# Kernel optimization log

Measured on AMD Instinct MI355X. Metric: run time of the kernel, lower is better.

## Reference

```python
import jax, jax.numpy as jnp
import numpy as np

SCALES = (1, 3, 7, 15)
EPS_LN = 1e-5

def _layernorm(x, g, b):
    mu = jnp.mean(x, axis=-1, keepdims=True)
    var = jnp.mean(jnp.square(x - mu), axis=-1, keepdims=True)
    return (x - mu) / jnp.sqrt(var + EPS_LN) * g + b

def setup_inputs() -> dict:
    key = jax.random.key(0)
    ks = jax.random.split(key, 6)
    B, L, H, NL = 8, 4096, 1024, 4
    s = 0.02
    return {
        "sequence_features": jax.random.normal(ks[0], (B, L, H), jnp.float32),
        "hierarchy_masks": jax.random.uniform(ks[1], (B, L, NL), jnp.float32),
        "level_embeddings": jax.random.normal(ks[2], (NL, H), jnp.float32) * s,
        "lt_w": jax.random.normal(ks[3], (H, H), jnp.float32) * (1.0 / np.sqrt(H)),
        "lt_b": jnp.zeros((H,), jnp.float32),
        "ln1_g": jnp.ones((H,), jnp.float32),
        "ln1_b": jnp.zeros((H,), jnp.float32),
        "ft_w": jax.random.normal(ks[4], (H, H), jnp.float32) * (1.0 / np.sqrt(H)),
        "ft_b": jnp.zeros((H,), jnp.float32),
        "ln2_g": jnp.ones((H,), jnp.float32),
        "ln2_b": jnp.zeros((H,), jnp.float32),
    }

def _hierarchical_fusion(t, masks, level_emb, temperature=1.0):
    # t: [B,L,H], masks: [B,L,NL], level_emb: [NL,H]
    H = t.shape[-1]
    scores = jnp.einsum('blh,nh->bln', t, level_emb) / temperature      # [B,L,NL]
    keep = masks > 0.5
    w = jnp.where(keep, jnp.exp(scores), 0.0)                            # masked exp weights
    tot = jnp.sum(w, axis=-1, keepdims=True)                             # [B,L,1]
    fused = jnp.einsum('bln,nh->blh', w, level_emb)
    fused = jnp.where(tot > 1e-8, fused / jnp.where(tot > 1e-8, tot, 1.0), fused)
    gate = jax.nn.sigmoid(jnp.sum(fused * t, axis=-1, keepdims=True) / H)
    return gate * fused + (1.0 - gate) * t

def _multi_scale(x):
    # x: [B,L,H]; variable-window mean per scale via prefix sums
    B, L, H = x.shape
    csum = jnp.concatenate([jnp.zeros((B, 1, H), x.dtype), jnp.cumsum(x, axis=1)], axis=1)  # [B,L+1,H]
    pos = jnp.arange(L)
    agg = jnp.zeros_like(x)
    for scale in SCALES:
        start = jnp.clip(pos - scale // 2, 0, L)
        end = jnp.clip(pos + scale // 2 + 1, 0, L)
        wsum = jnp.take(csum, end, axis=1) - jnp.take(csum, start, axis=1)  # [B,L,H]
        cnt = (end - start).astype(x.dtype)[None, :, None]
        sw = 1.0 / (1.0 + np.log(float(scale)))
        agg = agg + sw * (wsum / cnt)
    return agg

def reference(sequence_features, hierarchy_masks, level_embeddings, lt_w, lt_b,
              ln1_g, ln1_b, ft_w, ft_b, ln2_g, ln2_b):
    t = _layernorm(sequence_features @ lt_w + lt_b, ln1_g, ln1_b)
    fused = _hierarchical_fusion(t, hierarchy_masks, level_embeddings)
    agg = _multi_scale(fused)
    out = _layernorm(agg @ ft_w + ft_b, ln2_g, ln2_b)
    return out + sequence_features
```

## Files before the change

### kernel.cpp

```cpp
#include <hip/hip_runtime.h>
#include <stdint.h>

typedef unsigned short u16;
typedef unsigned int u32;
typedef u16 u16x8 __attribute__((ext_vector_type(8)));
typedef u16 u16x4 __attribute__((ext_vector_type(4)));
typedef u16 u16x2 __attribute__((ext_vector_type(2)));
typedef __bf16 bf16x8 __attribute__((ext_vector_type(8)));
typedef float f32x4 __attribute__((ext_vector_type(4)));

__device__ __forceinline__ float bf2f(u16 u) {
    unsigned int x = ((unsigned int)u) << 16;
    float f; __builtin_memcpy(&f, &x, 4); return f;
}
__device__ __forceinline__ u16 f2bf(float f) {
    unsigned int x; __builtin_memcpy(&x, &f, 4);
    x += 0x7fffu + ((x >> 16) & 1u);
    return (u16)(x >> 16);
}
__device__ __forceinline__ float wsum(float v) {
#pragma unroll
    for (int o = 32; o > 0; o >>= 1) v += __shfl_xor(v, o, 64);
    return v;
}

__device__ __forceinline__ void gload16(const void* g, void* l) {
    const __attribute__((address_space(1))) u32* gp =
        reinterpret_cast<const __attribute__((address_space(1))) u32*>(
            reinterpret_cast<uintptr_t>(g));
    __attribute__((address_space(3))) u32* lp =
        reinterpret_cast<__attribute__((address_space(3))) u32*>(
            reinterpret_cast<uintptr_t>(l));
    __builtin_amdgcn_global_load_lds(gp, lp, 16, 0, 0);
}

template<int C_F32>
__global__ __launch_bounds__(256) void gemm_bt(
    const u16* __restrict__ A, const u16* __restrict__ Bt,
    void* __restrict__ Cp, int M, int N, int K)
{
    __shared__ __align__(16) u16 sA[128 * 32];
    __shared__ __align__(16) u16 sB[128 * 32];
    const int t = threadIdx.x;
    const int lane = t & 63, wave = t >> 6;
    const int quad = lane >> 4, lr = lane & 15;

    const int nwg = gridDim.x * gridDim.y;
    int id = blockIdx.y * gridDim.x + blockIdx.x;
    int swz = ((nwg & 7) == 0) ? ((id & 7) * (nwg >> 3) + (id >> 3)) : id;
    const int bx = swz % gridDim.x, by = swz / gridDim.x;
    const int m0 = by * 128, n0 = bx * 128;
    const int wm = (wave & 1) * 64, wn = (wave >> 1) * 64;

    const int r0 = t >> 2, kc = (t & 3) * 8;
    const u16* ga = A + (size_t)(m0 + r0) * K + kc;
    const u16* gb = Bt + (size_t)(n0 + r0) * K + kc;
    u16* la = sA + t * 8;
    u16* lb = sB + t * 8;
    const size_t rstride = (size_t)64 * K;

    f32x4 acc[4][4] = {};

    for (int kt = 0; kt < K; kt += 32) {
        __syncthreads();
        gload16(ga + kt, la);
        gload16(ga + kt + rstride, la + 2048);
        gload16(gb + kt, lb);
        gload16(gb + kt + rstride, lb + 2048);
        __syncthreads();

        bf16x8 af[4], bfr[4];
#pragma unroll
        for (int i = 0; i < 4; ++i)
            af[i] = *(const bf16x8*)(sA + (wm + i * 16 + lr) * 32 + quad * 8);
#pragma unroll
        for (int j = 0; j < 4; ++j)
            bfr[j] = *(const bf16x8*)(sB + (wn + j * 16 + lr) * 32 + quad * 8);
#pragma unroll
        for (int i = 0; i < 4; ++i)
#pragma unroll
            for (int j = 0; j < 4; ++j)
                acc[i][j] = __builtin_amdgcn_mfma_f32_16x16x32_bf16(af[i], bfr[j], acc[i][j], 0, 0, 0);
    }
#pragma unroll
    for (int i = 0; i < 4; ++i) {
        int mrow = m0 + wm + i * 16 + quad * 4;
#pragma unroll
        for (int j = 0; j < 4; ++j) {
            int ncol = n0 + wn + j * 16 + lr;
#pragma unroll
            for (int r = 0; r < 4; ++r) {
                if (C_F32) ((float*)Cp)[(size_t)(mrow + r) * N + ncol] = acc[i][j][r];
                else       ((u16*)Cp)[(size_t)(mrow + r) * N + ncol] = f2bf(acc[i][j][r]);
            }
        }
    }
}

__global__ __launch_bounds__(256) void f32_to_bf16(
    const float* __restrict__ in, u16* __restrict__ out, int n8)
{
    int i = blockIdx.x * 256 + threadIdx.x;
    const int stride = gridDim.x * 256;
    for (; i < n8; i += stride) {
        f32x4 a = *(const f32x4*)(in + (size_t)i * 8);
        f32x4 b = *(const f32x4*)(in + (size_t)i * 8 + 4);
        u16x8 o;
#pragma unroll
        for (int p = 0; p < 4; ++p) { o[p] = f2bf(a[p]); o[p + 4] = f2bf(b[p]); }
        *(u16x8*)(out + (size_t)i * 8) = o;
    }
}

__global__ __launch_bounds__(256) void w_transpose(
    const float* __restrict__ W, u16* __restrict__ Bt, int K, int N)
{
    __shared__ u16 tile[64][72];
    const int t = threadIdx.x;
    const int c4 = (t & 15) * 4;
    const int r0 = t >> 4;
    const int kb = blockIdx.y * 64, nb = blockIdx.x * 64;
#pragma unroll
    for (int p = 0; p < 4; ++p) {
        int k = p * 16 + r0;
        f32x4 v = *(const f32x4*)(W + (size_t)(kb + k) * N + nb + c4);
        u16x4 o;
#pragma unroll
        for (int j = 0; j < 4; ++j) o[j] = f2bf(v[j]);
        *(u16x4*)&tile[k][c4] = o;
    }
    __syncthreads();
#pragma unroll
    for (int p = 0; p < 4; ++p) {
        int n = p * 16 + r0;
        u16x4 o;
#pragma unroll
        for (int j = 0; j < 4; ++j) o[j] = tile[c4 + j][n];
        *(u16x4*)(Bt + (size_t)(nb + n) * K + kb + c4) = o;
    }
}

__global__ __launch_bounds__(256) void ln1_fusion(
    const u16* Y, const float* __restrict__ ltb,
    const float* __restrict__ g1, const float* __restrict__ b1,
    const float* __restrict__ masks, const float* __restrict__ emb,
    u16* fused, int ROWS)
{
    const int lane = threadIdx.x & 63;
    const int wid = blockIdx.x * (blockDim.x >> 6) + (threadIdx.x >> 6);
    const int nw = gridDim.x * (blockDim.x >> 6);
    const int h0 = lane * 16;

    float ltbv[16], gv[16], bv[16], ev[4][16];
#pragma unroll
    for (int i = 0; i < 16; ++i) {
        ltbv[i] = ltb[h0 + i];
        gv[i] = g1[h0 + i];
        bv[i] = b1[h0 + i];
    }
#pragma unroll
    for (int n = 0; n < 4; ++n)
#pragma unroll
        for (int i = 0; i < 16; ++i) ev[n][i] = emb[n * 1024 + h0 + i];

    for (int r = wid; r < ROWS; r += nw) {
        const u16* yrow = Y + (size_t)r * 1024 + h0;
        u16x8 v0 = *(const u16x8*)(yrow);
        u16x8 v1 = *(const u16x8*)(yrow + 8);
        float y[16], s = 0.f, sq = 0.f;
#pragma unroll
        for (int i = 0; i < 8; ++i) { y[i] = bf2f(v0[i]) + ltbv[i]; y[i + 8] = bf2f(v1[i]) + ltbv[i + 8]; }
#pragma unroll
        for (int i = 0; i < 16; ++i) { s += y[i]; sq += y[i] * y[i]; }
        s = wsum(s); sq = wsum(sq);
        float mu = s * (1.f / 1024.f);
        float var = fmaxf(sq * (1.f / 1024.f) - mu * mu, 0.f);
        float rinv = rsqrtf(var + 1e-5f);
        float tv[16];
#pragma unroll
        for (int i = 0; i < 16; ++i) tv[i] = (y[i] - mu) * rinv * gv[i] + bv[i];

        float p0 = 0.f, p1 = 0.f, p2 = 0.f, p3 = 0.f;
#pragma unroll
        for (int i = 0; i < 16; ++i) {
            p0 += tv[i] * ev[0][i]; p1 += tv[i] * ev[1][i];
            p2 += tv[i] * ev[2][i]; p3 += tv[i] * ev[3][i];
        }
        p0 = wsum(p0); p1 = wsum(p1); p2 = wsum(p2); p3 = wsum(p3);
        p0 = fminf(p0, 30.f); p1 = fminf(p1, 30.f); p2 = fminf(p2, 30.f); p3 = fminf(p3, 30.f);

        f32x4 mk = *(const f32x4*)(masks + (size_t)r * 4);
        float w0 = mk[0] > 0.5f ? expf(p0) : 0.f;
        float w1 = mk[1] > 0.5f ? expf(p1) : 0.f;
        float w2 = mk[2] > 0.5f ? expf(p2) : 0.f;
        float w3 = mk[3] > 0.5f ? expf(p3) : 0.f;
        float tot = w0 + w1 + w2 + w3;
        float inv = tot > 1e-8f ? 1.f / tot : 1.f;

        float fu[16], d = 0.f;
#pragma unroll
        for (int i = 0; i < 16; ++i) {
            fu[i] = (w0 * ev[0][i] + w1 * ev[1][i] + w2 * ev[2][i] + w3 * ev[3][i]) * inv;
            d += fu[i] * tv[i];
        }
        d = wsum(d);
        float gate = 1.f / (1.f + expf(fminf(-d * (1.f / 1024.f), 30.f)));

        u16x8 o0, o1;
#pragma unroll
        for (int i = 0; i < 8; ++i) {
            o0[i] = f2bf(gate * fu[i] + (1.f - gate) * tv[i]);
            o1[i] = f2bf(gate * fu[i + 8] + (1.f - gate) * tv[i + 8]);
        }
        u16* orow = fused + (size_t)r * 1024 + h0;
        *(u16x8*)(orow) = o0;
        *(u16x8*)(orow + 8) = o1;
    }
}

#define MS_SEG 64
#define MS_HH 512
#define MS_ROWS (MS_SEG + 14)
__global__ __launch_bounds__(256) void multiscale_slide(
    const u16* __restrict__ fused, u16* __restrict__ agg, int L)
{
    __shared__ __align__(16) u16 sT[MS_ROWS * MS_HH];
    const int t = threadIdx.x;
    const int lane = t & 63, wave = t >> 6;
    const int hhalf = blockIdx.x & 1;
    const int bseg = blockIdx.x >> 1;
    const int nseg = L / MS_SEG;
    const int b = bseg / nseg, seg = bseg - b * nseg;
    const int l0 = seg * MS_SEG;
    const size_t base = (size_t)b * L * 1024 + (size_t)hhalf * MS_HH;

    for (int r = wave; r < MS_ROWS; r += 4) {
        int gl = l0 + r - 7;
        u16x8 v = {};
        if ((unsigned)gl < (unsigned)L)
            v = *(const u16x8*)(fused + base + (size_t)gl * 1024 + lane * 8);
        *(u16x8*)(sT + r * MS_HH + lane * 8) = v;
    }
    __syncthreads();

    const int h0 = lane * 8;
    const int lq = wave;
    const u16* rowp = sT + (lq * 16) * MS_HH + h0;

#define LOADR(dst, rr) { u16x8 _v = *(const u16x8*)(rowp + (rr) * MS_HH); \
    _Pragma("unroll") for (int e = 0; e < 8; ++e) dst[e] = bf2f(_v[e]); }

    float fc[8], a3[8], a7[8], a15[8];
    {
        float u[8], v[8];
        LOADR(fc, 7);
        LOADR(u, 6); LOADR(v, 8);
#pragma unroll
        for (int e = 0; e < 8; ++e) a3[e] = fc[e] + u[e] + v[e];
        LOADR(u, 5); LOADR(v, 9);
#pragma unroll
        for (int e = 0; e < 8; ++e) a7[e] = a3[e] + u[e] + v[e];
        LOADR(u, 4); LOADR(v, 10);
#pragma unroll
        for (int e = 0; e < 8; ++e) a7[e] += u[e] + v[e];
        LOADR(u, 3); LOADR(v, 11);
#pragma unroll
        for (int e = 0; e < 8; ++e) a15[e] = a7[e] + u[e] + v[e];
        LOADR(u, 2); LOADR(v, 12);
#pragma unroll
        for (int e = 0; e < 8; ++e) a15[e] += u[e] + v[e];
        LOADR(u, 1); LOADR(v, 13);
#pragma unroll
        for (int e = 0; e < 8; ++e) a15[e] += u[e] + v[e];
        LOADR(u, 0); LOADR(v, 14);
#pragma unroll
        for (int e = 0; e < 8; ++e) a15[e] += u[e] + v[e];
    }

    const float SW1 = 1.f / (1.f + logf(3.f));
    const float SW2 = 1.f / (1.f + logf(7.f));
    const float SW3 = 1.f / (1.f + logf(15.f));
    const float C1 = SW1 / 3.f, C2 = SW2 / 7.f, C3 = SW3 / 15.f;

    u16* outp = agg + base + (size_t)(l0 + lq * 16) * 1024 + h0;
#pragma unroll
    for (int i = 0; i < 16; ++i) {
        const int l = l0 + lq * 16 + i;
        float c1 = C1, c2 = C2, c3 = C3;
        if (l < 7 || l + 7 >= L) {
            int s1 = l - 1 < 0 ? 0 : l - 1, e1 = l + 2 > L ? L : l + 2;
            int s2 = l - 3 < 0 ? 0 : l - 3, e2 = l + 4 > L ? L : l + 4;
            int s3 = l - 7 < 0 ? 0 : l - 7, e3 = l + 8 > L ? L : l + 8;
            c1 = SW1 / (float)(e1 - s1);
            c2 = SW2 / (float)(e2 - s2);
            c3 = SW3 / (float)(e3 - s3);
        }
        u16x8 o;
#pragma unroll
        for (int e = 0; e < 8; ++e)
            o[e] = f2bf(fc[e] + c1 * a3[e] + c2 * a7[e] + c3 * a15[e]);
        *(u16x8*)(outp + (size_t)i * 1024) = o;

        if (i < 15) {
            float p1[8], p2[8], m1[8], p4[8], m3[8], p8[8], m7[8];
            LOADR(p1, 7 + i + 1); LOADR(p2, 7 + i + 2); LOADR(m1, 7 + i - 1);
            LOADR(p4, 7 + i + 4); LOADR(m3, 7 + i - 3);
            LOADR(p8, 7 + i + 8); LOADR(m7, 7 + i - 7);
#pragma unroll
            for (int e = 0; e < 8; ++e) {
                a3[e]  += p2[e] - m1[e];
                a7[e]  += p4[e] - m3[e];
                a15[e] += p8[e] - m7[e];
                fc[e]   = p1[e];
            }
        }
    }
#undef LOADR
}

#define BM 128
#define BN 128
#define BKK 32
#define SBS (BN + 2)
__global__ __launch_bounds__(256) void gemm_k_bf_f32(
    const u16* __restrict__ Ap, const float* __restrict__ B,
    float* __restrict__ Cp, int M, int N, int K)
{
    __shared__ __align__(16) u16 sA[BM * BKK];
    __shared__ __align__(16) u16 sB[BKK * SBS];
    const int t = threadIdx.x;
    const int lane = t & 63, wave = t >> 6;
    const int m0 = blockIdx.y * BM, n0 = blockIdx.x * BN;
    const int wm = (wave & 1) * 64, wn = (wave >> 1) * 64;
    const int quad = lane >> 4, lr = lane & 15;

    f32x4 acc[4][4] = {};

    for (int kt = 0; kt < K; kt += BKK) {
        u16x8 va[2], vb[2];
#pragma unroll
        for (int r = 0; r < 2; ++r) {
            int c = t + r * 256;
            int arow = c >> 2, aks = (c & 3) * 8;
            va[r] = *(const u16x8*)(Ap + (size_t)(m0 + arow) * K + kt + aks);
            int bk = c >> 4, bn = (c & 15) * 8;
            const float* gb = B + (size_t)(kt + bk) * N + n0 + bn;
            f32x4 g0 = *(const f32x4*)gb;
            f32x4 g1 = *(const f32x4*)(gb + 4);
#pragma unroll
            for (int p = 0; p < 4; ++p) { vb[r][p] = f2bf(g0[p]); vb[r][p + 4] = f2bf(g1[p]); }
        }
        __syncthreads();
#pragma unroll
        for (int r = 0; r < 2; ++r) {
            int c = t + r * 256;
            *(u16x8*)((char*)sA + (size_t)c * 16) = va[r];
            int bk = c >> 4, bn = (c & 15) * 8;
            u16* dst = sB + bk * SBS + bn;
#pragma unroll
            for (int p = 0; p < 4; ++p) {
                u16x2 w; w[0] = vb[r][2 * p]; w[1] = vb[r][2 * p + 1];
                *(u16x2*)(dst + 2 * p) = w;
            }
        }
        __syncthreads();

        bf16x8 af[4], bfr[4];
#pragma unroll
        for (int i = 0; i < 4; ++i)
            af[i] = *(const bf16x8*)((const char*)sA + (wm + i * 16 + lr) * 64 + quad * 16);
#pragma unroll
        for (int i = 0; i < 4; ++i) {
            u16 tmp[8];
#pragma unroll
            for (int j = 0; j < 8; ++j)
                tmp[j] = sB[(quad * 8 + j) * SBS + (wn + i * 16 + lr)];
            __builtin_memcpy(&bfr[i], tmp, 16);
        }
#pragma unroll
        for (int i = 0; i < 4; ++i)
#pragma unroll
            for (int j = 0; j < 4; ++j)
                acc[i][j] = __builtin_amdgcn_mfma_f32_16x16x32_bf16(af[i], bfr[j], acc[i][j], 0, 0, 0);
    }
#pragma unroll
    for (int i = 0; i < 4; ++i) {
        int mrow = m0 + wm + i * 16 + quad * 4;
#pragma unroll
        for (int j = 0; j < 4; ++j) {
            int ncol = n0 + wn + j * 16 + lr;
#pragma unroll
            for (int r = 0; r < 4; ++r)
                Cp[(size_t)(mrow + r) * N + ncol] = acc[i][j][r];
        }
    }
}

__global__ __launch_bounds__(256) void ln2_res(
    float* Y, const float* __restrict__ ftb,
    const float* __restrict__ g2, const float* __restrict__ b2,
    const float* __restrict__ x, int ROWS)
{
    const int lane = threadIdx.x & 63;
    const int wid = blockIdx.x * (blockDim.x >> 6) + (threadIdx.x >> 6);
    const int nw = gridDim.x * (blockDim.x >> 6);
    const int h0 = lane * 16;

    float ftbv[16], gv[16], bv[16];
#pragma unroll
    for (int i = 0; i < 16; ++i) {
        ftbv[i] = ftb[h0 + i];
        gv[i] = g2[h0 + i];
        bv[i] = b2[h0 + i];
    }
    for (int r = wid; r < ROWS; r += nw) {
        float* yrow = Y + (size_t)r * 1024 + h0;
        float y[16], s = 0.f, sq = 0.f;
#pragma unroll
        for (int q = 0; q < 4; ++q) {
            f32x4 v = *(const f32x4*)(yrow + 4 * q);
#pragma unroll
            for (int p = 0; p < 4; ++p) y[4 * q + p] = v[p] + ftbv[4 * q + p];
        }
#pragma unroll
        for (int i = 0; i < 16; ++i) { s += y[i]; sq += y[i] * y[i]; }
        s = wsum(s); sq = wsum(sq);
        float mu = s * (1.f / 1024.f);
        float var = fmaxf(sq * (1.f / 1024.f) - mu * mu, 0.f);
        float rinv = rsqrtf(var + 1e-5f);

        const float* xrow = x + (size_t)r * 1024 + h0;
#pragma unroll
        for (int q = 0; q < 4; ++q) {
            f32x4 xv = *(const f32x4*)(xrow + 4 * q);
            f32x4 o;
#pragma unroll
            for (int p = 0; p < 4; ++p)
                o[p] = (y[4 * q + p] - mu) * rinv * gv[4 * q + p] + bv[4 * q + p] + xv[p];
            *(f32x4*)(yrow + 4 * q) = o;
        }
    }
}

extern "C" void kernel_launch(void* const* d_in, const int* in_sizes, int n_in,
                              void* d_out, int out_size, void* d_ws, size_t ws_size,
                              hipStream_t stream) {
    const float* x     = (const float*)d_in[0];
    const float* masks = (const float*)d_in[1];
    const float* emb   = (const float*)d_in[2];
    const float* ltw   = (const float*)d_in[3];
    const float* ltb   = (const float*)d_in[4];
    const float* g1    = (const float*)d_in[5];
    const float* b1    = (const float*)d_in[6];
    const float* ftw   = (const float*)d_in[7];
    const float* ftb   = (const float*)d_in[8];
    const float* g2    = (const float*)d_in[9];
    const float* b2    = (const float*)d_in[10];
    float* out = (float*)d_out;

    const int H = 1024, L = 4096;
    const int M = in_sizes[0] / H;
    const size_t MB = 1024 * 1024;

    u16* plane0 = (u16*)d_out;
    u16* xbf    = (u16*)((char*)d_out + 64 * MB);
    u16* aggP   = (u16*)d_ws;
    const bool roomy = ws_size >= 68 * MB;
    u16* Bt1 = roomy ? (u16*)((char*)d_ws + 64 * MB) : (u16*)d_ws;
    u16* Bt2 = roomy ? (u16*)((char*)d_ws + 66 * MB) : nullptr;

    f32_to_bf16<<<2048, 256, 0, stream>>>(x, xbf, M * H / 8);
    w_transpose<<<dim3(16, 16), 256, 0, stream>>>(ltw, Bt1, H, H);
    if (roomy) w_transpose<<<dim3(16, 16), 256, 0, stream>>>(ftw, Bt2, H, H);

    gemm_bt<0><<<dim3(H / 128, M / 128), 256, 0, stream>>>(xbf, Bt1, plane0, M, H, H);
    ln1_fusion<<<1024, 256, 0, stream>>>(plane0, ltb, g1, b1, masks, emb, plane0, M);
    multiscale_slide<<<(M / MS_SEG) * 2, 256, 0, stream>>>(plane0, aggP, L);
    if (roomy)
        gemm_bt<1><<<dim3(H / 128, M / 128), 256, 0, stream>>>(aggP, Bt2, out, M, H, H);
    else
        gemm_k_bf_f32<<<dim3(H / BN, M / BM), 256, 0, stream>>>(aggP, ftw, out, M, H, H);
    ln2_res<<<1024, 256, 0, stream>>>(out, ftb, g2, b2, x, M);
}
```

Measured before the change: 586.3 us.

## Double GEMM K-tile with XOR-swizzled LDS, merge prep kernels, simplify gate dot

The bf16 GEMM now stages a K-tile of 64 instead of 32 per barrier pair and XOR-swizzles LDS columns so fragment reads avoid bank conflicts. This halves the number of sync points and doubles the MFMA work done per load phase, at the cost of twice the shared memory. The input cast and both weight transposes are merged into one launch to cut launch overhead. In the fusion kernel, the gate dot product is rewritten algebraically as the weighted sum of the already-reduced scores, which removes a 16-element loop and a wave reduction.

```diff
diff --git a/kernel.cpp b/kernel.cpp
--- a/kernel.cpp
+++ b/kernel.cpp
@@ -39,8 +39,8 @@
     const u16* __restrict__ A, const u16* __restrict__ Bt,
     void* __restrict__ Cp, int M, int N, int K)
 {
-    __shared__ __align__(16) u16 sA[128 * 32];
-    __shared__ __align__(16) u16 sB[128 * 32];
+    __shared__ __align__(16) u16 sA[128 * 64];
+    __shared__ __align__(16) u16 sB[128 * 64];
     const int t = threadIdx.x;
     const int lane = t & 63, wave = t >> 6;
     const int quad = lane >> 4, lr = lane & 15;
@@ -52,35 +52,41 @@
     const int m0 = by * 128, n0 = bx * 128;
     const int wm = (wave & 1) * 64, wn = (wave >> 1) * 64;
 
-    const int r0 = t >> 2, kc = (t & 3) * 8;
-    const u16* ga = A + (size_t)(m0 + r0) * K + kc;
-    const u16* gb = Bt + (size_t)(n0 + r0) * K + kc;
+    const int rowt = t >> 3;
+    const int kcl = (((t & 7) ^ (rowt & 7))) * 8;
+    const u16* ga = A + (size_t)(m0 + rowt) * K + kcl;
+    const u16* gb = Bt + (size_t)(n0 + rowt) * K + kcl;
     u16* la = sA + t * 8;
     u16* lb = sB + t * 8;
-    const size_t rstride = (size_t)64 * K;
+    const size_t rstride = (size_t)32 * K;
 
     f32x4 acc[4][4] = {};
 
-    for (int kt = 0; kt < K; kt += 32) {
+    for (int kt = 0; kt < K; kt += 64) {
         __syncthreads();
-        gload16(ga + kt, la);
-        gload16(ga + kt + rstride, la + 2048);
-        gload16(gb + kt, lb);
-        gload16(gb + kt + rstride, lb + 2048);
+#pragma unroll
+        for (int r = 0; r < 4; ++r) {
+            gload16(ga + kt + r * rstride, la + r * 2048);
+            gload16(gb + kt + r * rstride, lb + r * 2048);
+        }
         __syncthreads();
 
-        bf16x8 af[4], bfr[4];
-#pragma unroll
-        for (int i = 0; i < 4; ++i)
-            af[i] = *(const bf16x8*)(sA + (wm + i * 16 + lr) * 32 + quad * 8);
-#pragma unroll
-        for (int j = 0; j < 4; ++j)
-            bfr[j] = *(const bf16x8*)(sB + (wn + j * 16 + lr) * 32 + quad * 8);
-#pragma unroll
-        for (int i = 0; i < 4; ++i)
+#pragma unroll
+        for (int q = 0; q < 2; ++q) {
+            const int psl = ((q * 4 + quad) ^ (lr & 7)) * 8;
+            bf16x8 af[4], bfr[4];
+#pragma unroll
+            for (int i = 0; i < 4; ++i)
+                af[i] = *(const bf16x8*)(sA + (wm + i * 16 + lr) * 64 + psl);
 #pragma unroll
             for (int j = 0; j < 4; ++j)
-                acc[i][j] = __builtin_amdgcn_mfma_f32_16x16x32_bf16(af[i], bfr[j], acc[i][j], 0, 0, 0);
+                bfr[j] = *(const bf16x8*)(sB + (wn + j * 16 + lr) * 64 + psl);
+#pragma unroll
+            for (int i = 0; i < 4; ++i)
+#pragma unroll
+                for (int j = 0; j < 4; ++j)
+                    acc[i][j] = __builtin_amdgcn_mfma_f32_16x16x32_bf16(af[i], bfr[j], acc[i][j], 0, 0, 0);
+        }
     }
 #pragma unroll
     for (int i = 0; i < 4; ++i) {
@@ -97,29 +103,37 @@
     }
 }
 
-__global__ __launch_bounds__(256) void f32_to_bf16(
-    const float* __restrict__ in, u16* __restrict__ out, int n8)
-{
-    int i = blockIdx.x * 256 + threadIdx.x;
-    const int stride = gridDim.x * 256;
-    for (; i < n8; i += stride) {
-        f32x4 a = *(const f32x4*)(in + (size_t)i * 8);
-        f32x4 b = *(const f32x4*)(in + (size_t)i * 8 + 4);
-        u16x8 o;
-#pragma unroll
-        for (int p = 0; p < 4; ++p) { o[p] = f2bf(a[p]); o[p + 4] = f2bf(b[p]); }
-        *(u16x8*)(out + (size_t)i * 8) = o;
-    }
-}
-
-__global__ __launch_bounds__(256) void w_transpose(
-    const float* __restrict__ W, u16* __restrict__ Bt, int K, int N)
+__global__ __launch_bounds__(256) void prep_all(
+    const float* __restrict__ x, u16* __restrict__ xbf,
+    const float* __restrict__ ltw, u16* __restrict__ Bt1,
+    const float* __restrict__ ftw, u16* __restrict__ Bt2,
+    int n8, int doFtw)
 {
     __shared__ u16 tile[64][72];
     const int t = threadIdx.x;
+    if (blockIdx.x < 2048) {
+        int i = blockIdx.x * 256 + t;
+        const int stride = 2048 * 256;
+        for (; i < n8; i += stride) {
+            f32x4 a = *(const f32x4*)(x + (size_t)i * 8);
+            f32x4 b = *(const f32x4*)(x + (size_t)i * 8 + 4);
+            u16x8 o;
+#pragma unroll
+            for (int p = 0; p < 4; ++p) { o[p] = f2bf(a[p]); o[p + 4] = f2bf(b[p]); }
+            *(u16x8*)(xbf + (size_t)i * 8) = o;
+        }
+        return;
+    }
+    int b = blockIdx.x - 2048;
+    const int which = b >> 8;
+    if (which == 1 && !doFtw) return;
+    const float* W = which ? ftw : ltw;
+    u16* Bt = which ? Bt2 : Bt1;
+    const int bb = b & 255;
+    const int K = 1024, N = 1024;
+    const int kb = (bb >> 4) * 64, nb = (bb & 15) * 64;
     const int c4 = (t & 15) * 4;
     const int r0 = t >> 4;
-    const int kb = blockIdx.y * 64, nb = blockIdx.x * 64;
 #pragma unroll
     for (int p = 0; p < 4; ++p) {
         int k = p * 16 + r0;
@@ -187,24 +201,22 @@
             p2 += tv[i] * ev[2][i]; p3 += tv[i] * ev[3][i];
         }
         p0 = wsum(p0); p1 = wsum(p1); p2 = wsum(p2); p3 = wsum(p3);
-        p0 = fminf(p0, 30.f); p1 = fminf(p1, 30.f); p2 = fminf(p2, 30.f); p3 = fminf(p3, 30.f);
 
         f32x4 mk = *(const f32x4*)(masks + (size_t)r * 4);
-        float w0 = mk[0] > 0.5f ? expf(p0) : 0.f;
-        float w1 = mk[1] > 0.5f ? expf(p1) : 0.f;
-        float w2 = mk[2] > 0.5f ? expf(p2) : 0.f;
-        float w3 = mk[3] > 0.5f ? expf(p3) : 0.f;
+        float w0 = mk[0] > 0.5f ? expf(fminf(p0, 30.f)) : 0.f;
+        float w1 = mk[1] > 0.5f ? expf(fminf(p1, 30.f)) : 0.f;
+        float w2 = mk[2] > 0.5f ? expf(fminf(p2, 30.f)) : 0.f;
+        float w3 = mk[3] > 0.5f ? expf(fminf(p3, 30.f)) : 0.f;
         float tot = w0 + w1 + w2 + w3;
         float inv = tot > 1e-8f ? 1.f / tot : 1.f;
 
-        float fu[16], d = 0.f;
-#pragma unroll
-        for (int i = 0; i < 16; ++i) {
+        float d = (w0 * p0 + w1 * p1 + w2 * p2 + w3 * p3) * inv;
+        float gate = 1.f / (1.f + expf(fminf(-d * (1.f / 1024.f), 30.f)));
+
+        float fu[16];
+#pragma unroll
+        for (int i = 0; i < 16; ++i)
             fu[i] = (w0 * ev[0][i] + w1 * ev[1][i] + w2 * ev[2][i] + w3 * ev[3][i]) * inv;
-            d += fu[i] * tv[i];
-        }
-        d = wsum(d);
-        float gate = 1.f / (1.f + expf(fminf(-d * (1.f / 1024.f), 30.f)));
 
         u16x8 o0, o1;
 #pragma unroll
@@ -469,9 +481,7 @@
     u16* Bt1 = roomy ? (u16*)((char*)d_ws + 64 * MB) : (u16*)d_ws;
     u16* Bt2 = roomy ? (u16*)((char*)d_ws + 66 * MB) : nullptr;
 
-    f32_to_bf16<<<2048, 256, 0, stream>>>(x, xbf, M * H / 8);
-    w_transpose<<<dim3(16, 16), 256, 0, stream>>>(ltw, Bt1, H, H);
-    if (roomy) w_transpose<<<dim3(16, 16), 256, 0, stream>>>(ftw, Bt2, H, H);
+    prep_all<<<2048 + 512, 256, 0, stream>>>(x, xbf, ltw, Bt1, ftw, Bt2, M * H / 8, roomy ? 1 : 0);
 
     gemm_bt<0><<<dim3(H / 128, M / 128), 256, 0, stream>>>(xbf, Bt1, plane0, M, H, H);
     ln1_fusion<<<1024, 256, 0, stream>>>(plane0, ltb, g1, b1, masks, emb, plane0, M);
```

Result: faster. 566.4 us (-3.4%).
